# Kernel optimization log

Hardware: AMD Instinct MI355X
Metric: run time of the kernel (lower is better)

The kernel has to match this reference:

```python
import jax, jax.numpy as jnp
import numpy as np

B, S, D, H = 4, 2048, 512, 8
DEPTH = D // H
BAND = 16  # log_thresholds [1,2,4,8,16] union == distance <= 16


def setup_inputs() -> dict:
    key = jax.random.key(0)
    ks = jax.random.split(key, 11)
    sc = 0.02
    return {
        "q": jax.random.normal(ks[0], (B, S, D), jnp.float32),
        "k": jax.random.normal(ks[1], (B, S, D), jnp.float32),
        "v": jax.random.normal(ks[2], (B, S, D), jnp.float32),
        "wq": jax.random.normal(ks[3], (D, D), jnp.float32) * sc,
        "bq": jnp.zeros((D,), jnp.float32),
        "wk": jax.random.normal(ks[4], (D, D), jnp.float32) * sc,
        "bk": jnp.zeros((D,), jnp.float32),
        "wv": jax.random.normal(ks[5], (D, D), jnp.float32) * sc,
        "bv": jnp.zeros((D,), jnp.float32),
        "wo": jax.random.normal(ks[6], (D, D), jnp.float32) * sc,
        "bo": jnp.zeros((D,), jnp.float32),
    }


def _split_heads(x):
    # [B,S,D] -> [B,H,S,depth]
    b, s, _ = x.shape
    return x.reshape(b, s, H, DEPTH).transpose(0, 2, 1, 3)


def reference(q, k, v, wq, bq, wk, bk, wv, bv, wo, bo):
    qh = _split_heads(q @ wq + bq)
    kh = _split_heads(k @ wk + bk)
    vh = _split_heads(v @ wv + bv)
    scale = 1.0 / jnp.sqrt(jnp.float32(DEPTH))
    logits = jnp.einsum("bhqd,bhkd->bhqk", qh, kh) * scale  # [B,H,S,S]
    idx = jnp.arange(S)
    keep = jnp.abs(idx[:, None] - idx[None, :]) <= BAND  # band mask [S,S]
    logits = jnp.where(keep[None, None], logits, jnp.float32(-1e9))
    attn = jax.nn.softmax(logits, axis=-1)
    out = jnp.einsum("bhqk,bhkd->bhqd", attn, vh)
    out = out.transpose(0, 2, 1, 3).reshape(q.shape[0], -1, D)
    return out @ wo + bo
```

## Files before the change

kernel.cpp:

```cpp
#include <hip/hip_runtime.h>

typedef unsigned int uint;
typedef unsigned short ushort;
typedef __attribute__((ext_vector_type(8))) short bf16x8;
typedef __attribute__((ext_vector_type(4))) float f32x4;

namespace {
constexpr int kS = 2048;
constexpr int kD = 512;
constexpr int kH = 8;
constexpr int kNT = 8192;
constexpr int kBand = 16;
}

static __device__ __forceinline__ ushort f2bf(float f) {
  uint u = __builtin_bit_cast(uint, f);
  u = (u + 0x7fffu + ((u >> 16) & 1u)) >> 16;
  return (ushort)u;
}

#define GLD16(gp, lp)                                                   \
  __builtin_amdgcn_global_load_lds(                                     \
      (const __attribute__((address_space(1))) uint*)(gp),              \
      (__attribute__((address_space(3))) uint*)(lp), 16, 0, 0)

__global__ __launch_bounds__(256) void prep_kernel(
    const float* __restrict__ q, const float* __restrict__ k,
    const float* __restrict__ v, const float* __restrict__ wq,
    const float* __restrict__ wk, const float* __restrict__ wv,
    const float* __restrict__ wo, ushort* __restrict__ qb,
    ushort* __restrict__ kb, ushort* __restrict__ vb,
    ushort* __restrict__ WT) {
  __shared__ float Ws[64][65];
  const int blk = blockIdx.x;
  const int tid = threadIdx.x;
  if (blk < 6144) {
    const int z = blk >> 11, t = blk & 2047;
    const float* src = z == 0 ? q : (z == 1 ? k : v);
    ushort* dst = z == 0 ? qb : (z == 1 ? kb : vb);
    const size_t i8 = ((size_t)t * 256 + tid) * 8;
    const float4 x0 = *(const float4*)(src + i8);
    const float4 x1 = *(const float4*)(src + i8 + 4);
    alignas(16) ushort t8[8] = {f2bf(x0.x), f2bf(x0.y), f2bf(x0.z), f2bf(x0.w),
                                f2bf(x1.x), f2bf(x1.y), f2bf(x1.z), f2bf(x1.w)};
    *(uint4*)(dst + i8) = *(const uint4*)t8;
    return;
  }
  const int w = blk - 6144;
  const int z = w >> 6;
  const float* W = z == 0 ? wq : (z == 1 ? wk : (z == 2 ? wv : wo));
  ushort* T = WT + (size_t)z * kD * kD;
  const int kt = ((w >> 3) & 7) * 64, nt = (w & 7) * 64;
  const int r = tid >> 2, c0 = (tid & 3) * 16;
#pragma unroll
  for (int i = 0; i < 4; ++i) {
    const float4 x =
        *(const float4*)(W + (size_t)(kt + r) * kD + nt + c0 + i * 4);
    Ws[r][c0 + i * 4 + 0] = x.x;
    Ws[r][c0 + i * 4 + 1] = x.y;
    Ws[r][c0 + i * 4 + 2] = x.z;
    Ws[r][c0 + i * 4 + 3] = x.w;
  }
  __syncthreads();
  const int n = tid >> 2, k0 = (tid & 3) * 16;
  alignas(16) ushort tmp[16];
#pragma unroll
  for (int i = 0; i < 16; ++i) tmp[i] = f2bf(Ws[k0 + i][n]);
  ushort* dst = T + (size_t)(nt + n) * kD + kt + k0;
  *(uint4*)(dst + 0) = *(const uint4*)&tmp[0];
  *(uint4*)(dst + 8) = *(const uint4*)&tmp[8];
}

__global__ __launch_bounds__(256) void gemm_kernel(
    const ushort* __restrict__ qb, const ushort* __restrict__ kb,
    const ushort* __restrict__ vb, const ushort* __restrict__ obp,
    const ushort* __restrict__ WT, const float* __restrict__ bq,
    const float* __restrict__ bk, const float* __restrict__ bv,
    const float* __restrict__ bo, ushort* __restrict__ Qp,
    ushort* __restrict__ Kp, ushort* __restrict__ VT,
    float* __restrict__ outp, int mode_arg) {
  const int mode = mode_arg + blockIdx.z;
  const ushort* Ab;
  const float* bias;
  switch (mode) {
    case 0: Ab = qb; bias = bq; break;
    case 1: Ab = kb; bias = bk; break;
    case 2: Ab = vb; bias = bv; break;
    default: Ab = obp; bias = bo; break;
  }
  const ushort* BT = WT + (size_t)mode * kD * kD;

  __shared__ alignas(16) ushort smem[24576];

  const int tid = threadIdx.x;
  const int wave = tid >> 6, lane = tid & 63, l15 = lane & 15, qd = lane >> 4;
  const int wm = (wave >> 1) * 64, wn = (wave & 1) * 64;
  const int row0 = blockIdx.y * 128, col0 = blockIdx.x * 128;
  const int sw = (l15 & 3) ^ (l15 >> 2);

  const ushort* pA[2];
  const ushort* pB[2];
  uint ldsA[2], ldsB[2];
#pragma unroll
  for (int i = 0; i < 2; ++i) {
    const int linear = i * 256 + tid;
    const int r = linear >> 2, c = linear & 3;
    const int g = c ^ ((r & 3) ^ ((r >> 2) & 3));
    pA[i] = Ab + (size_t)(row0 + r) * kD + g * 8;
    pB[i] = BT + (size_t)(col0 + r) * kD + g * 8;
    ldsA[i] = (uint)(i * 256 + wave * 64) * 8;
    ldsB[i] = 12288u + (uint)(i * 256 + wave * 64) * 8;
  }

#define ISSUE(kk, st)                                  \
  {                                                    \
    GLD16(pA[0] + (kk), &smem[ldsA[0] + (st) * 4096]); \
    GLD16(pA[1] + (kk), &smem[ldsA[1] + (st) * 4096]); \
    GLD16(pB[0] + (kk), &smem[ldsB[0] + (st) * 4096]); \
    GLD16(pB[1] + (kk), &smem[ldsB[1] + (st) * 4096]); \
  }

  f32x4 acc[4][4];
#pragma unroll
  for (int mi = 0; mi < 4; ++mi)
#pragma unroll
    for (int ni = 0; ni < 4; ++ni) acc[mi][ni] = (f32x4)(0.f);

  ISSUE(0, 0);
  ISSUE(32, 1);
#pragma unroll
  for (int it = 0; it < 16; ++it) {
    if (it < 15)
      asm volatile("s_waitcnt vmcnt(4) lgkmcnt(0)\n\ts_barrier" ::: "memory");
    else
      asm volatile("s_waitcnt vmcnt(0) lgkmcnt(0)\n\ts_barrier" ::: "memory");
    if (it < 14) ISSUE((it + 2) * 32, (it + 2) % 3);
    const ushort* as = &smem[(it % 3) * 4096];
    const ushort* bs = &smem[12288 + (it % 3) * 4096];
    bf16x8 af[4], br[4];
#pragma unroll
    for (int mi = 0; mi < 4; ++mi)
      af[mi] = *(const bf16x8*)&as[(wm + mi * 16 + l15) * 32 + (qd ^ sw) * 8];
#pragma unroll
    for (int ni = 0; ni < 4; ++ni)
      br[ni] = *(const bf16x8*)&bs[(wn + ni * 16 + l15) * 32 + (qd ^ sw) * 8];
#pragma unroll
    for (int mi = 0; mi < 4; ++mi)
#pragma unroll
      for (int ni = 0; ni < 4; ++ni)
        acc[mi][ni] = __builtin_amdgcn_mfma_f32_16x16x32_bf16(
            af[mi], br[ni], acc[mi][ni], 0, 0, 0);
  }
#undef ISSUE

  __syncthreads();

  float bcol[4];
#pragma unroll
  for (int ni = 0; ni < 4; ++ni) bcol[ni] = bias[col0 + wn + ni * 16 + l15];

  if (mode == 3) {
#pragma unroll
    for (int mi = 0; mi < 4; ++mi)
#pragma unroll
      for (int ni = 0; ni < 4; ++ni) {
        const int n_g = col0 + wn + ni * 16 + l15;
#pragma unroll
        for (int r = 0; r < 4; ++r) {
          const int token = row0 + wm + mi * 16 + qd * 4 + r;
          outp[(size_t)token * kD + n_g] = acc[mi][ni][r] + bcol[ni];
        }
      }
    return;
  }

  ushort* T = &smem[wave * 4608];
  if (mode <= 1) {
#pragma unroll
    for (int mi = 0; mi < 4; ++mi)
#pragma unroll
      for (int ni = 0; ni < 4; ++ni)
#pragma unroll
        for (int r = 0; r < 4; ++r)
          T[(mi * 16 + qd * 4 + r) * 72 + ni * 16 + l15] =
              f2bf(acc[mi][ni][r] + bcol[ni]);
  } else {
#pragma unroll
    for (int mi = 0; mi < 4; ++mi)
#pragma unroll
      for (int ni = 0; ni < 4; ++ni)
#pragma unroll
        for (int r = 0; r < 4; ++r)
          T[(ni * 16 + l15) * 72 + mi * 16 + qd * 4 + r] =
              f2bf(acc[mi][ni][r] + bcol[ni]);
  }
  asm volatile("s_waitcnt lgkmcnt(0)" ::: "memory");

  const ushort* Trow = &smem[wave * 4608 + lane * 72];
  if (mode <= 1) {
    ushort* C = (mode == 0) ? Qp : Kp;
    ushort* dst = C + (size_t)(row0 + wm + lane) * kD + col0 + wn;
#pragma unroll
    for (int c = 0; c < 8; ++c)
      *(uint4*)(dst + c * 8) = *(const uint4*)(Trow + c * 8);
  } else {
    const int n_g = col0 + wn + lane;
    const int h = n_g >> 6, d = n_g & 63;
    const int t0 = row0 + wm;
    const int b = t0 >> 11, ss = t0 & (kS - 1);
    ushort* dst = VT + ((size_t)(b * kH + h) * 64 + d) * kS + ss;
#pragma unroll
    for (int c = 0; c < 8; ++c)
      *(uint4*)(dst + c * 8) = *(const uint4*)(Trow + c * 8);
  }
}

__global__ __launch_bounds__(64, 1) void attn_kernel(
    const ushort* __restrict__ Qp, const ushort* __restrict__ Kp,
    const ushort* __restrict__ VT, ushort* __restrict__ Ob) {
  __shared__ alignas(16) ushort Pl[64 * 104];

  const int lane = threadIdx.x, l15 = lane & 15, qd = lane >> 4;
  const int bh = blockIdx.y, b = bh >> 3, h = bh & 7;
  const int q0 = blockIdx.x * 64;
  const int colA = h * 64;

  bf16x8 qf[4][2], kf[6][2];
#pragma unroll
  for (int mi = 0; mi < 4; ++mi) {
    const size_t base =
        ((size_t)b * kS + q0 + mi * 16 + l15) * kD + colA + qd * 8;
#pragma unroll
    for (int kc = 0; kc < 2; ++kc)
      qf[mi][kc] = *(const bf16x8*)&Qp[base + kc * 32];
  }
#pragma unroll
  for (int ni = 0; ni < 6; ++ni) {
    int key = q0 - kBand + ni * 16 + l15;
    key = key < 0 ? 0 : (key > kS - 1 ? kS - 1 : key);
    const size_t base = ((size_t)b * kS + key) * kD + colA + qd * 8;
#pragma unroll
    for (int kc = 0; kc < 2; ++kc)
      kf[ni][kc] = *(const bf16x8*)&Kp[base + kc * 32];
  }

  f32x4 S[4][6];
#pragma unroll
  for (int mi = 0; mi < 4; ++mi)
#pragma unroll
    for (int ni = 0; ni < 6; ++ni) S[mi][ni] = (f32x4)(0.f);
#pragma unroll
  for (int mi = 0; mi < 4; ++mi)
#pragma unroll
    for (int ni = 0; ni < 6; ++ni)
#pragma unroll
      for (int kc = 0; kc < 2; ++kc)
        S[mi][ni] = __builtin_amdgcn_mfma_f32_16x16x32_bf16(
            qf[mi][kc], kf[ni][kc], S[mi][ni], 0, 0, 0);

#pragma unroll
  for (int mi = 0; mi < 4; ++mi)
#pragma unroll
    for (int ni = 0; ni < 6; ++ni)
#pragma unroll
      for (int r = 0; r < 4; ++r) {
        const int q_local = mi * 16 + qd * 4 + r;
        const int key_local = ni * 16 + l15;
        const int key = q0 - kBand + key_local;
        const int dlt = key_local - q_local;
        const bool ok = (dlt >= 0) && (dlt <= 32) && (key >= 0) && (key < kS);
        S[mi][ni][r] = ok ? S[mi][ni][r] * 0.125f : -3.0e38f;
      }

  float inv[4][4];
#pragma unroll
  for (int mi = 0; mi < 4; ++mi)
#pragma unroll
    for (int r = 0; r < 4; ++r) {
      float m = S[mi][0][r];
#pragma unroll
      for (int ni = 1; ni < 6; ++ni) m = fmaxf(m, S[mi][ni][r]);
      m = fmaxf(m, __shfl_xor(m, 1));
      m = fmaxf(m, __shfl_xor(m, 2));
      m = fmaxf(m, __shfl_xor(m, 4));
      m = fmaxf(m, __shfl_xor(m, 8));
      float s = 0.f;
#pragma unroll
      for (int ni = 0; ni < 6; ++ni) {
        const float e = __expf(S[mi][ni][r] - m);
        S[mi][ni][r] = e;
        s += e;
      }
      s += __shfl_xor(s, 1);
      s += __shfl_xor(s, 2);
      s += __shfl_xor(s, 4);
      s += __shfl_xor(s, 8);
      inv[mi][r] = 1.f / s;
    }

#pragma unroll
  for (int mi = 0; mi < 4; ++mi)
#pragma unroll
    for (int ni = 0; ni < 6; ++ni)
#pragma unroll
      for (int r = 0; r < 4; ++r)
        Pl[(mi * 16 + qd * 4 + r) * 104 + ni * 16 + l15] = f2bf(S[mi][ni][r]);
  __syncthreads();

  f32x4 O[4][4];
#pragma unroll
  for (int mi = 0; mi < 4; ++mi)
#pragma unroll
    for (int nt = 0; nt < 4; ++nt) O[mi][nt] = (f32x4)(0.f);

#pragma unroll
  for (int kc = 0; kc < 3; ++kc) {
    bf16x8 pf[4], vfr[4];
#pragma unroll
    for (int mi = 0; mi < 4; ++mi)
      pf[mi] = *(const bf16x8*)&Pl[(mi * 16 + l15) * 104 + kc * 32 + qd * 8];
    int kb0 = q0 - kBand + kc * 32 + qd * 8;
    kb0 = kb0 < 0 ? 0 : (kb0 > kS - 8 ? kS - 8 : kb0);
#pragma unroll
    for (int nt = 0; nt < 4; ++nt)
      vfr[nt] =
          *(const bf16x8*)&VT[((size_t)bh * 64 + nt * 16 + l15) * kS + kb0];
#pragma unroll
    for (int mi = 0; mi < 4; ++mi)
#pragma unroll
      for (int nt = 0; nt < 4; ++nt)
        O[mi][nt] = __builtin_amdgcn_mfma_f32_16x16x32_bf16(pf[mi], vfr[nt],
                                                            O[mi][nt], 0, 0, 0);
  }

#pragma unroll
  for (int mi = 0; mi < 4; ++mi)
#pragma unroll
    for (int nt = 0; nt < 4; ++nt)
#pragma unroll
      for (int r = 0; r < 4; ++r)
        Pl[(mi * 16 + qd * 4 + r) * 72 + nt * 16 + l15] =
            f2bf(O[mi][nt][r] * inv[mi][r]);
  asm volatile("s_waitcnt lgkmcnt(0)" ::: "memory");

  ushort* dst = Ob + ((size_t)b * kS + q0 + lane) * kD + colA;
  const ushort* Trow = &Pl[lane * 72];
#pragma unroll
  for (int c = 0; c < 8; ++c)
    *(uint4*)(dst + c * 8) = *(const uint4*)(Trow + c * 8);
}

extern "C" void kernel_launch(void* const* d_in, const int* in_sizes, int n_in,
                              void* d_out, int out_size, void* d_ws,
                              size_t ws_size, hipStream_t stream) {
  const float* q = (const float*)d_in[0];
  const float* k = (const float*)d_in[1];
  const float* v = (const float*)d_in[2];
  const float* wq = (const float*)d_in[3];
  const float* bq = (const float*)d_in[4];
  const float* wk = (const float*)d_in[5];
  const float* bk = (const float*)d_in[6];
  const float* wv = (const float*)d_in[7];
  const float* bv = (const float*)d_in[8];
  const float* wo = (const float*)d_in[9];
  const float* bo = (const float*)d_in[10];
  float* out = (float*)d_out;

  ushort* qb = (ushort*)d_ws;
  ushort* kb = qb + (size_t)kNT * kD;
  ushort* vb = kb + (size_t)kNT * kD;
  ushort* Kp = vb + (size_t)kNT * kD;
  ushort* VT = Kp + (size_t)kNT * kD;
  ushort* WT = VT + (size_t)kNT * kD;
  ushort* Qp = vb;
  ushort* Ob = kb;

  prep_kernel<<<dim3(6400), 256, 0, stream>>>(q, k, v, wq, wk, wv, wo, qb, kb,
                                              vb, WT);
  gemm_kernel<<<dim3(4, 64, 2), 256, 0, stream>>>(
      qb, kb, vb, Ob, WT, bq, bk, bv, bo, Qp, Kp, VT, out, 1);
  gemm_kernel<<<dim3(4, 64, 1), 256, 0, stream>>>(
      qb, kb, vb, Ob, WT, bq, bk, bv, bo, Qp, Kp, VT, out, 0);
  attn_kernel<<<dim3(kS / 64, 32), 64, 0, stream>>>(Qp, Kp, VT, Ob);
  gemm_kernel<<<dim3(4, 64, 1), 256, 0, stream>>>(
      qb, kb, vb, Ob, WT, bq, bk, bv, bo, Qp, Kp, VT, out, 3);
}
```

Before: 170.3 us.

## Merge QKV projections into one launch and use 64-row tiles for output GEMM

```diff
diff --git a/kernel.cpp b/kernel.cpp
--- a/kernel.cpp
+++ b/kernel.cpp
@@ -71,6 +71,7 @@
   *(uint4*)(dst + 8) = *(const uint4*)&tmp[8];
 }
 
+template <int TM>
 __global__ __launch_bounds__(256) void gemm_kernel(
     const ushort* __restrict__ qb, const ushort* __restrict__ kb,
     const ushort* __restrict__ vb, const ushort* __restrict__ obp,
@@ -90,80 +91,93 @@
   }
   const ushort* BT = WT + (size_t)mode * kD * kD;
 
-  __shared__ alignas(16) ushort smem[24576];
+  constexpr int A_STAGE = TM * 32;
+  constexpr int B_BASE = 3 * A_STAGE;
+  constexpr int NI = (TM == 128) ? 4 : 2;
+  constexpr int AI = TM / 64;
+  __shared__ alignas(16) ushort smem[B_BASE + 12288];
 
   const int tid = threadIdx.x;
   const int wave = tid >> 6, lane = tid & 63, l15 = lane & 15, qd = lane >> 4;
-  const int wm = (wave >> 1) * 64, wn = (wave & 1) * 64;
-  const int row0 = blockIdx.y * 128, col0 = blockIdx.x * 128;
+  const int wm = (TM == 128) ? (wave >> 1) * 64 : 0;
+  const int wn = (TM == 128) ? (wave & 1) * 64 : wave * 32;
+  const int row0 = blockIdx.y * TM, col0 = blockIdx.x * 128;
   const int sw = (l15 & 3) ^ (l15 >> 2);
 
-  const ushort* pA[2];
+  const ushort* pA[AI];
   const ushort* pB[2];
-  uint ldsA[2], ldsB[2];
+  uint ldsA[AI], ldsB[2];
+#pragma unroll
+  for (int i = 0; i < AI; ++i) {
+    const int linear = i * 256 + tid;
+    const int r = linear >> 2, c = linear & 3;
+    const int g = c ^ ((r & 3) ^ ((r >> 2) & 3));
+    pA[i] = Ab + (size_t)(row0 + r) * kD + g * 8;
+    ldsA[i] = (uint)(i * 256 + wave * 64) * 8;
+  }
 #pragma unroll
   for (int i = 0; i < 2; ++i) {
     const int linear = i * 256 + tid;
     const int r = linear >> 2, c = linear & 3;
     const int g = c ^ ((r & 3) ^ ((r >> 2) & 3));
-    pA[i] = Ab + (size_t)(row0 + r) * kD + g * 8;
     pB[i] = BT + (size_t)(col0 + r) * kD + g * 8;
-    ldsA[i] = (uint)(i * 256 + wave * 64) * 8;
-    ldsB[i] = 12288u + (uint)(i * 256 + wave * 64) * 8;
-  }
-
-#define ISSUE(kk, st)                                  \
-  {                                                    \
-    GLD16(pA[0] + (kk), &smem[ldsA[0] + (st) * 4096]); \
-    GLD16(pA[1] + (kk), &smem[ldsA[1] + (st) * 4096]); \
-    GLD16(pB[0] + (kk), &smem[ldsB[0] + (st) * 4096]); \
-    GLD16(pB[1] + (kk), &smem[ldsB[1] + (st) * 4096]); \
-  }
-
-  f32x4 acc[4][4];
-#pragma unroll
-  for (int mi = 0; mi < 4; ++mi)
-#pragma unroll
-    for (int ni = 0; ni < 4; ++ni) acc[mi][ni] = (f32x4)(0.f);
+    ldsB[i] = (uint)B_BASE + (uint)(i * 256 + wave * 64) * 8;
+  }
+
+#define ISSUE(kk, st)                                                     \
+  {                                                                       \
+    _Pragma("unroll") for (int i = 0; i < AI; ++i)                        \
+        GLD16(pA[i] + (kk), &smem[ldsA[i] + (st) * A_STAGE]);             \
+    _Pragma("unroll") for (int i = 0; i < 2; ++i)                         \
+        GLD16(pB[i] + (kk), &smem[ldsB[i] + (st) * 4096]);                \
+  }
+
+  f32x4 acc[4][NI];
+#pragma unroll
+  for (int mi = 0; mi < 4; ++mi)
+#pragma unroll
+    for (int ni = 0; ni < NI; ++ni) acc[mi][ni] = (f32x4)(0.f);
 
   ISSUE(0, 0);
   ISSUE(32, 1);
 #pragma unroll
   for (int it = 0; it < 16; ++it) {
-    if (it < 15)
-      asm volatile("s_waitcnt vmcnt(4) lgkmcnt(0)\n\ts_barrier" ::: "memory");
-    else
+    if (it < 15) {
+      if constexpr (TM == 128)
+        asm volatile("s_waitcnt vmcnt(4) lgkmcnt(0)\n\ts_barrier" ::: "memory");
+      else
+        asm volatile("s_waitcnt vmcnt(3) lgkmcnt(0)\n\ts_barrier" ::: "memory");
+    } else {
       asm volatile("s_waitcnt vmcnt(0) lgkmcnt(0)\n\ts_barrier" ::: "memory");
+    }
     if (it < 14) ISSUE((it + 2) * 32, (it + 2) % 3);
-    const ushort* as = &smem[(it % 3) * 4096];
-    const ushort* bs = &smem[12288 + (it % 3) * 4096];
-    bf16x8 af[4], br[4];
+    const ushort* as = &smem[(it % 3) * A_STAGE];
+    const ushort* bs = &smem[B_BASE + (it % 3) * 4096];
+    bf16x8 af[4], br[NI];
 #pragma unroll
     for (int mi = 0; mi < 4; ++mi)
       af[mi] = *(const bf16x8*)&as[(wm + mi * 16 + l15) * 32 + (qd ^ sw) * 8];
 #pragma unroll
-    for (int ni = 0; ni < 4; ++ni)
+    for (int ni = 0; ni < NI; ++ni)
       br[ni] = *(const bf16x8*)&bs[(wn + ni * 16 + l15) * 32 + (qd ^ sw) * 8];
 #pragma unroll
     for (int mi = 0; mi < 4; ++mi)
 #pragma unroll
-      for (int ni = 0; ni < 4; ++ni)
+      for (int ni = 0; ni < NI; ++ni)
         acc[mi][ni] = __builtin_amdgcn_mfma_f32_16x16x32_bf16(
             af[mi], br[ni], acc[mi][ni], 0, 0, 0);
   }
 #undef ISSUE
 
-  __syncthreads();
-
-  float bcol[4];
-#pragma unroll
-  for (int ni = 0; ni < 4; ++ni) bcol[ni] = bias[col0 + wn + ni * 16 + l15];
+  float bcol[NI];
+#pragma unroll
+  for (int ni = 0; ni < NI; ++ni) bcol[ni] = bias[col0 + wn + ni * 16 + l15];
 
   if (mode == 3) {
 #pragma unroll
     for (int mi = 0; mi < 4; ++mi)
 #pragma unroll
-      for (int ni = 0; ni < 4; ++ni) {
+      for (int ni = 0; ni < NI; ++ni) {
         const int n_g = col0 + wn + ni * 16 + l15;
 #pragma unroll
         for (int r = 0; r < 4; ++r) {
@@ -174,12 +188,14 @@
     return;
   }
 
+  __syncthreads();
+
   ushort* T = &smem[wave * 4608];
   if (mode <= 1) {
 #pragma unroll
     for (int mi = 0; mi < 4; ++mi)
 #pragma unroll
-      for (int ni = 0; ni < 4; ++ni)
+      for (int ni = 0; ni < NI; ++ni)
 #pragma unroll
         for (int r = 0; r < 4; ++r)
           T[(mi * 16 + qd * 4 + r) * 72 + ni * 16 + l15] =
@@ -188,7 +204,7 @@
 #pragma unroll
     for (int mi = 0; mi < 4; ++mi)
 #pragma unroll
-      for (int ni = 0; ni < 4; ++ni)
+      for (int ni = 0; ni < NI; ++ni)
 #pragma unroll
         for (int r = 0; r < 4; ++r)
           T[(ni * 16 + l15) * 72 + mi * 16 + qd * 4 + r] =
@@ -366,22 +382,21 @@
   const float* bo = (const float*)d_in[10];
   float* out = (float*)d_out;
 
+  const size_t n1 = (size_t)kNT * kD;
   ushort* qb = (ushort*)d_ws;
-  ushort* kb = qb + (size_t)kNT * kD;
-  ushort* vb = kb + (size_t)kNT * kD;
-  ushort* Kp = vb + (size_t)kNT * kD;
-  ushort* VT = Kp + (size_t)kNT * kD;
-  ushort* WT = VT + (size_t)kNT * kD;
-  ushort* Qp = vb;
-  ushort* Ob = kb;
+  ushort* kb = qb + n1;
+  ushort* vb = kb + n1;
+  ushort* Qp = vb + n1;
+  ushort* Kp = Qp + n1;
+  ushort* VT = Kp + n1;
+  ushort* Ob = VT + n1;
+  ushort* WT = Ob + n1;
 
   prep_kernel<<<dim3(6400), 256, 0, stream>>>(q, k, v, wq, wk, wv, wo, qb, kb,
                                               vb, WT);
-  gemm_kernel<<<dim3(4, 64, 2), 256, 0, stream>>>(
-      qb, kb, vb, Ob, WT, bq, bk, bv, bo, Qp, Kp, VT, out, 1);
-  gemm_kernel<<<dim3(4, 64, 1), 256, 0, stream>>>(
+  gemm_kernel<128><<<dim3(4, 64, 3), 256, 0, stream>>>(
       qb, kb, vb, Ob, WT, bq, bk, bv, bo, Qp, Kp, VT, out, 0);
   attn_kernel<<<dim3(kS / 64, 32), 64, 0, stream>>>(Qp, Kp, VT, Ob);
-  gemm_kernel<<<dim3(4, 64, 1), 256, 0, stream>>>(
+  gemm_kernel<64><<<dim3(4, 128, 1), 256, 0, stream>>>(
       qb, kb, vb, Ob, WT, bq, bk, bv, bo, Qp, Kp, VT, out, 3);
 }
```

New measurement: 161.8 us. 5.0% less time.

## Fuse fp32-to-bf16 input conversion into GEMM with direct global fragment loads

Applied to the files above, without the earlier changes.

```diff
diff --git a/kernel.cpp b/kernel.cpp
--- a/kernel.cpp
+++ b/kernel.cpp
@@ -19,34 +19,13 @@
   return (ushort)u;
 }
 
-#define GLD16(gp, lp)                                                   \
-  __builtin_amdgcn_global_load_lds(                                     \
-      (const __attribute__((address_space(1))) uint*)(gp),              \
-      (__attribute__((address_space(3))) uint*)(lp), 16, 0, 0)
-
-__global__ __launch_bounds__(256) void prep_kernel(
-    const float* __restrict__ q, const float* __restrict__ k,
-    const float* __restrict__ v, const float* __restrict__ wq,
-    const float* __restrict__ wk, const float* __restrict__ wv,
-    const float* __restrict__ wo, ushort* __restrict__ qb,
-    ushort* __restrict__ kb, ushort* __restrict__ vb,
+__global__ __launch_bounds__(256) void prep_w_kernel(
+    const float* __restrict__ wq, const float* __restrict__ wk,
+    const float* __restrict__ wv, const float* __restrict__ wo,
     ushort* __restrict__ WT) {
   __shared__ float Ws[64][65];
-  const int blk = blockIdx.x;
+  const int w = blockIdx.x;
   const int tid = threadIdx.x;
-  if (blk < 6144) {
-    const int z = blk >> 11, t = blk & 2047;
-    const float* src = z == 0 ? q : (z == 1 ? k : v);
-    ushort* dst = z == 0 ? qb : (z == 1 ? kb : vb);
-    const size_t i8 = ((size_t)t * 256 + tid) * 8;
-    const float4 x0 = *(const float4*)(src + i8);
-    const float4 x1 = *(const float4*)(src + i8 + 4);
-    alignas(16) ushort t8[8] = {f2bf(x0.x), f2bf(x0.y), f2bf(x0.z), f2bf(x0.w),
-                                f2bf(x1.x), f2bf(x1.y), f2bf(x1.z), f2bf(x1.w)};
-    *(uint4*)(dst + i8) = *(const uint4*)t8;
-    return;
-  }
-  const int w = blk - 6144;
   const int z = w >> 6;
   const float* W = z == 0 ? wq : (z == 1 ? wk : (z == 2 ? wv : wo));
   ushort* T = WT + (size_t)z * kD * kD;
@@ -71,54 +50,51 @@
   *(uint4*)(dst + 8) = *(const uint4*)&tmp[8];
 }
 
+template <bool F32A>
 __global__ __launch_bounds__(256) void gemm_kernel(
-    const ushort* __restrict__ qb, const ushort* __restrict__ kb,
-    const ushort* __restrict__ vb, const ushort* __restrict__ obp,
+    const float* __restrict__ qf, const float* __restrict__ kf,
+    const float* __restrict__ vf, const ushort* __restrict__ obp,
     const ushort* __restrict__ WT, const float* __restrict__ bq,
     const float* __restrict__ bk, const float* __restrict__ bv,
     const float* __restrict__ bo, ushort* __restrict__ Qp,
     ushort* __restrict__ Kp, ushort* __restrict__ VT,
     float* __restrict__ outp, int mode_arg) {
   const int mode = mode_arg + blockIdx.z;
-  const ushort* Ab;
+  const float* Af = nullptr;
+  const ushort* Ab = nullptr;
   const float* bias;
   switch (mode) {
-    case 0: Ab = qb; bias = bq; break;
-    case 1: Ab = kb; bias = bk; break;
-    case 2: Ab = vb; bias = bv; break;
+    case 0: Af = qf; bias = bq; break;
+    case 1: Af = kf; bias = bk; break;
+    case 2: Af = vf; bias = bv; break;
     default: Ab = obp; bias = bo; break;
   }
   const ushort* BT = WT + (size_t)mode * kD * kD;
 
-  __shared__ alignas(16) ushort smem[24576];
+  __shared__ alignas(16) ushort smem[18432];
 
   const int tid = threadIdx.x;
   const int wave = tid >> 6, lane = tid & 63, l15 = lane & 15, qd = lane >> 4;
   const int wm = (wave >> 1) * 64, wn = (wave & 1) * 64;
-  const int row0 = blockIdx.y * 128, col0 = blockIdx.x * 128;
-  const int sw = (l15 & 3) ^ (l15 >> 2);
-
-  const ushort* pA[2];
-  const ushort* pB[2];
-  uint ldsA[2], ldsB[2];
-#pragma unroll
-  for (int i = 0; i < 2; ++i) {
-    const int linear = i * 256 + tid;
-    const int r = linear >> 2, c = linear & 3;
-    const int g = c ^ ((r & 3) ^ ((r >> 2) & 3));
-    pA[i] = Ab + (size_t)(row0 + r) * kD + g * 8;
-    pB[i] = BT + (size_t)(col0 + r) * kD + g * 8;
-    ldsA[i] = (uint)(i * 256 + wave * 64) * 8;
-    ldsB[i] = 12288u + (uint)(i * 256 + wave * 64) * 8;
-  }
-
-#define ISSUE(kk, st)                                  \
-  {                                                    \
-    GLD16(pA[0] + (kk), &smem[ldsA[0] + (st) * 4096]); \
-    GLD16(pA[1] + (kk), &smem[ldsA[1] + (st) * 4096]); \
-    GLD16(pB[0] + (kk), &smem[ldsB[0] + (st) * 4096]); \
-    GLD16(pB[1] + (kk), &smem[ldsB[1] + (st) * 4096]); \
-  }
+  const int lin = blockIdx.x;
+  const int xcd = lin & 7, j = lin >> 3;
+  const int rblk = xcd + 8 * (j >> 2), cblk = j & 3;
+  const int row0 = rblk * 128, col0 = cblk * 128;
+
+  const float* aF[4];
+  const ushort* aB[4];
+  const ushort* bP[4];
+#pragma unroll
+  for (int mi = 0; mi < 4; ++mi) {
+    const int row = row0 + wm + mi * 16 + l15;
+    if constexpr (F32A)
+      aF[mi] = Af + (size_t)row * kD + qd * 8;
+    else
+      aB[mi] = Ab + (size_t)row * kD + qd * 8;
+  }
+#pragma unroll
+  for (int ni = 0; ni < 4; ++ni)
+    bP[ni] = BT + (size_t)(col0 + wn + ni * 16 + l15) * kD + qd * 8;
 
   f32x4 acc[4][4];
 #pragma unroll
@@ -126,24 +102,31 @@
 #pragma unroll
     for (int ni = 0; ni < 4; ++ni) acc[mi][ni] = (f32x4)(0.f);
 
-  ISSUE(0, 0);
-  ISSUE(32, 1);
-#pragma unroll
-  for (int it = 0; it < 16; ++it) {
-    if (it < 15)
-      asm volatile("s_waitcnt vmcnt(4) lgkmcnt(0)\n\ts_barrier" ::: "memory");
-    else
-      asm volatile("s_waitcnt vmcnt(0) lgkmcnt(0)\n\ts_barrier" ::: "memory");
-    if (it < 14) ISSUE((it + 2) * 32, (it + 2) % 3);
-    const ushort* as = &smem[(it % 3) * 4096];
-    const ushort* bs = &smem[12288 + (it % 3) * 4096];
+#pragma unroll 2
+  for (int k0 = 0; k0 < kD; k0 += 32) {
     bf16x8 af[4], br[4];
 #pragma unroll
-    for (int mi = 0; mi < 4; ++mi)
-      af[mi] = *(const bf16x8*)&as[(wm + mi * 16 + l15) * 32 + (qd ^ sw) * 8];
-#pragma unroll
-    for (int ni = 0; ni < 4; ++ni)
-      br[ni] = *(const bf16x8*)&bs[(wn + ni * 16 + l15) * 32 + (qd ^ sw) * 8];
+    for (int ni = 0; ni < 4; ++ni) br[ni] = *(const bf16x8*)(bP[ni] + k0);
+    if constexpr (F32A) {
+#pragma unroll
+      for (int mi = 0; mi < 4; ++mi) {
+        const float4 x0 = *(const float4*)(aF[mi] + k0);
+        const float4 x1 = *(const float4*)(aF[mi] + k0 + 4);
+        bf16x8 t;
+        t[0] = (short)f2bf(x0.x);
+        t[1] = (short)f2bf(x0.y);
+        t[2] = (short)f2bf(x0.z);
+        t[3] = (short)f2bf(x0.w);
+        t[4] = (short)f2bf(x1.x);
+        t[5] = (short)f2bf(x1.y);
+        t[6] = (short)f2bf(x1.z);
+        t[7] = (short)f2bf(x1.w);
+        af[mi] = t;
+      }
+    } else {
+#pragma unroll
+      for (int mi = 0; mi < 4; ++mi) af[mi] = *(const bf16x8*)(aB[mi] + k0);
+    }
 #pragma unroll
     for (int mi = 0; mi < 4; ++mi)
 #pragma unroll
@@ -151,9 +134,6 @@
         acc[mi][ni] = __builtin_amdgcn_mfma_f32_16x16x32_bf16(
             af[mi], br[ni], acc[mi][ni], 0, 0, 0);
   }
-#undef ISSUE
-
-  __syncthreads();
 
   float bcol[4];
 #pragma unroll
@@ -366,22 +346,17 @@
   const float* bo = (const float*)d_in[10];
   float* out = (float*)d_out;
 
-  ushort* qb = (ushort*)d_ws;
-  ushort* kb = qb + (size_t)kNT * kD;
-  ushort* vb = kb + (size_t)kNT * kD;
-  ushort* Kp = vb + (size_t)kNT * kD;
-  ushort* VT = Kp + (size_t)kNT * kD;
-  ushort* WT = VT + (size_t)kNT * kD;
-  ushort* Qp = vb;
-  ushort* Ob = kb;
-
-  prep_kernel<<<dim3(6400), 256, 0, stream>>>(q, k, v, wq, wk, wv, wo, qb, kb,
-                                              vb, WT);
-  gemm_kernel<<<dim3(4, 64, 2), 256, 0, stream>>>(
-      qb, kb, vb, Ob, WT, bq, bk, bv, bo, Qp, Kp, VT, out, 1);
-  gemm_kernel<<<dim3(4, 64, 1), 256, 0, stream>>>(
-      qb, kb, vb, Ob, WT, bq, bk, bv, bo, Qp, Kp, VT, out, 0);
+  const size_t n1 = (size_t)kNT * kD;
+  ushort* Qp = (ushort*)d_ws;
+  ushort* Kp = Qp + n1;
+  ushort* VT = Kp + n1;
+  ushort* Ob = VT + n1;
+  ushort* WT = Ob + n1;
+
+  prep_w_kernel<<<dim3(256), 256, 0, stream>>>(wq, wk, wv, wo, WT);
+  gemm_kernel<true><<<dim3(256, 1, 3), 256, 0, stream>>>(
+      q, k, v, Ob, WT, bq, bk, bv, bo, Qp, Kp, VT, out, 0);
   attn_kernel<<<dim3(kS / 64, 32), 64, 0, stream>>>(Qp, Kp, VT, Ob);
-  gemm_kernel<<<dim3(4, 64, 1), 256, 0, stream>>>(
-      qb, kb, vb, Ob, WT, bq, bk, bv, bo, Qp, Kp, VT, out, 3);
-}
+  gemm_kernel<false><<<dim3(256, 1, 1), 256, 0, stream>>>(
+      q, k, v, Ob, WT, bq, bk, bv, bo, Qp, Kp, VT, out, 3);
+}
```

Result: slower. 208.9 us (+22.7%).
